# Performance work log

Measured on AMD Instinct MI355X. Metric: run time of the kernel, lower is better.

Reference implementation:

```python
import jax, jax.numpy as jnp
import numpy as np

B, T, N, D, H, C = 128, 128, 16, 128, 128, 4096
LEAKY_SLOPE = 0.2  # tf.nn.leaky_relu default alpha


def setup_inputs() -> dict:
    key = jax.random.key(0)
    ks = jax.random.split(key, 16)
    def p(k, shape, scale=0.05):
        return jax.random.normal(k, shape, dtype=jnp.float32) * scale
    return {
        "x_embed": jax.random.normal(ks[0], (B, T, D), dtype=jnp.float32),
        "spat_neigh": jax.random.normal(ks[1], (B, T, N, D), dtype=jnp.float32),
        "temp_neigh": jax.random.normal(ks[2], (B, T, N, D), dtype=jnp.float32),
        # spatial GAT params: shared projection w (no bias), attentionDense (2D->D, bias)
        "s_w": p(ks[3], (D, D)), "s_ak": p(ks[4], (2 * D, D)), "s_ab": jnp.zeros((D,), jnp.float32),
        # temporal GAT params
        "t_w": p(ks[5], (D, D)), "t_ak": p(ks[6], (2 * D, D)), "t_ab": jnp.zeros((D,), jnp.float32),
        # LSTMCell: W(x), U(h)+bias, s_W(spatial), t_W(temporal), each -> 4H
        "Wx": p(ks[7], (D, 4 * H)), "Uh": p(ks[8], (H, 4 * H)), "Ub": jnp.zeros((4 * H,), jnp.float32),
        "sW": p(ks[9], (D, 4 * H)), "tW": p(ks[10], (D, 4 * H)),
        # fuseDense -> num_classes
        "Wf": p(ks[11], (H, C)), "bf": jnp.zeros((C,), jnp.float32),
    }


def _gat(x, neigh, w, ak, ab):
    # x: [B,T,D], neigh: [B,T,N,D]
    px = x @ w                                   # projected main node [B,T,D]
    pn = neigh @ w                               # projected neighbours [B,T,N,D]
    cat = jnp.concatenate(
        [jnp.broadcast_to(px[:, :, None, :], pn.shape), pn], axis=-1)  # [B,T,N,2D]
    e = jax.nn.leaky_relu(cat @ ak + ab, negative_slope=LEAKY_SLOPE)   # [B,T,N,D]
    a = jax.nn.softmax(e, axis=2)                # softmax over neighbour axis
    return jnp.sum(a * pn, axis=2)               # [B,T,D]


def reference(x_embed, spat_neigh, temp_neigh,
              s_w, s_ak, s_ab, t_w, t_ak, t_ab,
              Wx, Uh, Ub, sW, tW, Wf, bf):
    spatial = _gat(x_embed, spat_neigh, s_w, s_ak, s_ab)   # [B,T,D]
    temporal = _gat(x_embed, temp_neigh, t_w, t_ak, t_ab)  # [B,T,D]

    # precompute non-recurrent gate preactivations for all timesteps
    pre = x_embed @ Wx + spatial @ sW + temporal @ tW + Ub  # [B,T,4H]
    pre_t = jnp.transpose(pre, (1, 0, 2))                   # [T,B,4H]

    def step(carry, p):
        h, c = carry
        g = p + h @ Uh                                      # [B,4H]
        i_g, f_g, o_g, c_g = jnp.split(g, 4, axis=-1)
        c = jax.nn.sigmoid(f_g) * c + jax.nn.sigmoid(i_g) * jnp.tanh(c_g)
        h = jnp.tanh(jax.nn.sigmoid(o_g) * c)  # nonstandard: tanh(o * c), per source
        return (h, c), h

    init = (jnp.zeros((B, H), jnp.float32), jnp.zeros((B, H), jnp.float32))
    _, hs = jax.lax.scan(step, init, pre_t)                 # [T,B,H]
    outputs = jnp.transpose(hs, (1, 0, 2))                  # [B,T,H]
    return outputs @ Wf + bf                                # [B,T,C] logits
```

## Files before the change

### kernel.cpp

```cpp
#include <hip/hip_runtime.h>
#include <hip/hip_bf16.h>
#include <math.h>

#define BT   16384
#define CC   4096

typedef __attribute__((ext_vector_type(8))) short short8v;
typedef __attribute__((ext_vector_type(8))) unsigned short ushort8v;
typedef __attribute__((ext_vector_type(4))) float f32x4;
typedef __attribute__((ext_vector_type(2))) _Float16 h2v;

__device__ __forceinline__ unsigned short f2bf(float f) {
  union { float f; unsigned int u; } v; v.f = f;
  unsigned int r = (v.u + 0x7fffu + ((v.u >> 16) & 1u)) >> 16;
  return (unsigned short)r;
}

__device__ __forceinline__ float fsig(float x) {
  return 1.0f / (1.0f + __expf(-x));
}
__device__ __forceinline__ float ftanh(float x) {
  return 1.0f - 2.0f / (__expf(2.0f * x) + 1.0f);
}

__device__ __forceinline__ float dot2f(float hbits, unsigned int ubits,
                                       float acc) {
#if __has_builtin(__builtin_amdgcn_fdot2)
  h2v ha = __builtin_bit_cast(h2v, hbits);
  h2v ub = __builtin_bit_cast(h2v, ubits);
  return __builtin_amdgcn_fdot2(ha, ub, acc, false);
#else
  union { unsigned int u; _Float16 h[2]; } A, B;
  A.u = __builtin_bit_cast(unsigned int, hbits);
  B.u = ubits;
  return acc + (float)A.h[0] * (float)B.h[0] + (float)A.h[1] * (float)B.h[1];
#endif
}

__global__ __launch_bounds__(128) void prep_dots_kernel(
    const float* __restrict__ s_w, const float* __restrict__ s_ak,
    const float* __restrict__ s_ab, const float* __restrict__ t_w,
    const float* __restrict__ t_ak, const float* __restrict__ t_ab,
    unsigned short* __restrict__ wqT, unsigned short* __restrict__ wcT,
    float* __restrict__ abp) {
  int d = blockIdx.x, quad = blockIdx.y;
  int g = quad & 1;
  const float* w  = g ? t_w  : s_w;
  const float* ak = g ? t_ak : s_ak;
  int akoff = (quad >> 1) ? 128 : 0;
  __shared__ float akcol[128];
  int k = threadIdx.x;
  akcol[k] = ak[(akoff + k) * 128 + d];
  if (quad < 2) {
    wcT[g * 32768 + d * 128 + k] = f2bf(w[k * 128 + d]);
    if (k == 0) abp[g * 128 + d] = g ? t_ab[d] : s_ab[d];
  }
  __syncthreads();
  float acc = 0.f;
  #pragma unroll 8
  for (int m = 0; m < 128; ++m) acc = fmaf(w[k * 128 + m], akcol[m], acc);
  if (quad < 2) wqT[(g * 128 + d) * 128 + k] = f2bf(acc);
  else          wcT[g * 32768 + (128 + d) * 128 + k] = f2bf(acc);
}

__global__ __launch_bounds__(256) void prep_wfT_kernel(
    const float* __restrict__ Wf, unsigned short* __restrict__ WfT) {
  __shared__ float tile[32][33];
  int n0 = blockIdx.x * 32, k0 = blockIdx.y * 32;
  int c = threadIdx.x & 31, r0 = threadIdx.x >> 5;
  #pragma unroll
  for (int i = 0; i < 4; ++i) {
    int r = r0 + i * 8;
    tile[r][c] = Wf[(size_t)(k0 + r) * 4096 + n0 + c];
  }
  __syncthreads();
  #pragma unroll
  for (int i = 0; i < 4; ++i) {
    int r = r0 + i * 8;
    WfT[(size_t)(n0 + r) * 128 + k0 + c] = f2bf(tile[c][r]);
  }
}

__global__ __launch_bounds__(256) void tconv_kernel(
    const float* __restrict__ s0, const float* __restrict__ s1,
    const float* __restrict__ s2, unsigned short* __restrict__ d0,
    unsigned short* __restrict__ d1, unsigned short* __restrict__ d2, int N) {
  int z = blockIdx.z;
  const float* src = (z == 0) ? s0 : (z == 1) ? s1 : s2;
  unsigned short* dst = (z == 0) ? d0 : (z == 1) ? d1 : d2;
  __shared__ float tile[32][33];
  int n0 = blockIdx.x * 32, k0 = blockIdx.y * 32;
  int c = threadIdx.x & 31, r0 = threadIdx.x >> 5;
  #pragma unroll
  for (int i = 0; i < 4; ++i) {
    int r = r0 + i * 8;
    tile[r][c] = src[(size_t)(k0 + r) * N + n0 + c];
  }
  __syncthreads();
  #pragma unroll
  for (int i = 0; i < 4; ++i) {
    int r = r0 + i * 8;
    dst[(size_t)(n0 + r) * 128 + k0 + c] = f2bf(tile[c][r]);
  }
}

__global__ __launch_bounds__(256) void uhconv_kernel(
    const float* __restrict__ Uh, unsigned int* __restrict__ UhH) {
  int idx = blockIdx.x * 256 + threadIdx.x;
  int k2 = idx >> 9, j = idx & 511;
  float a = Uh[(size_t)(2 * k2) * 512 + j];
  float b = Uh[(size_t)(2 * k2 + 1) * 512 + j];
  union { _Float16 h[2]; unsigned int u; } p;
  p.h[0] = (_Float16)a;
  p.h[1] = (_Float16)b;
  UhH[idx] = p.u;
}

__global__ __launch_bounds__(256) void xconv_kernel(
    const float* __restrict__ x, unsigned short* __restrict__ xb) {
  int i = blockIdx.x * 256 + threadIdx.x;
  const float4* x4 = (const float4*)x;
  float4 a = x4[(size_t)i * 2], b = x4[(size_t)i * 2 + 1];
  ushort8v v;
  v[0] = f2bf(a.x); v[1] = f2bf(a.y); v[2] = f2bf(a.z); v[3] = f2bf(a.w);
  v[4] = f2bf(b.x); v[5] = f2bf(b.y); v[6] = f2bf(b.z); v[7] = f2bf(b.w);
  *(ushort8v*)(xb + (size_t)i * 8) = v;
}

__global__ __launch_bounds__(256) void mfma_gemm_kernel(
    const unsigned short* __restrict__ A, const unsigned short* __restrict__ BTm,
    const float* __restrict__ bias, float* __restrict__ C, int N) {
  __shared__ unsigned short As[128 * 128];
  __shared__ unsigned short Bs[64 * 128];
  int tid = threadIdx.x;
  int m0 = blockIdx.x * 128, n0 = blockIdx.y * 64;
  #pragma unroll
  for (int i = 0; i < 8; ++i) {
    int cix = i * 256 + tid, row = cix >> 4, ch = cix & 15;
    ushort8v v = *(const ushort8v*)(A + (size_t)(m0 + row) * 128 + ch * 8);
    *(ushort8v*)&As[row * 128 + ((ch ^ (row & 7)) << 3)] = v;
  }
  #pragma unroll
  for (int i = 0; i < 4; ++i) {
    int cix = i * 256 + tid, row = cix >> 4, ch = cix & 15;
    ushort8v v = *(const ushort8v*)(BTm + (size_t)(n0 + row) * 128 + ch * 8);
    *(ushort8v*)&Bs[row * 128 + ((ch ^ (row & 7)) << 3)] = v;
  }
  __syncthreads();
  int lane = tid & 63, w = tid >> 6;
  int col = lane & 15, grp = lane >> 4;

  f32x4 acc[2][4];
  #pragma unroll
  for (int tm = 0; tm < 2; ++tm)
    #pragma unroll
    for (int tn = 0; tn < 4; ++tn) acc[tm][tn] = (f32x4){0.f, 0.f, 0.f, 0.f};

  #pragma unroll
  for (int kk = 0; kk < 4; ++kk) {
    int ch = kk * 4 + grp;
    short8v af[2], bf[4];
    #pragma unroll
    for (int tm = 0; tm < 2; ++tm) {
      int row = w * 32 + tm * 16 + col;
      af[tm] = *(const short8v*)&As[row * 128 + ((ch ^ (row & 7)) << 3)];
    }
    #pragma unroll
    for (int tn = 0; tn < 4; ++tn) {
      int row = tn * 16 + col;
      bf[tn] = *(const short8v*)&Bs[row * 128 + ((ch ^ (row & 7)) << 3)];
    }
    #pragma unroll
    for (int tm = 0; tm < 2; ++tm)
      #pragma unroll
      for (int tn = 0; tn < 4; ++tn)
        acc[tm][tn] = __builtin_amdgcn_mfma_f32_16x16x32_bf16(af[tm], bf[tn],
                                                              acc[tm][tn], 0, 0, 0);
  }

  #pragma unroll
  for (int tm = 0; tm < 2; ++tm)
    #pragma unroll
    for (int tn = 0; tn < 4; ++tn) {
      int cg = n0 + tn * 16 + col;
      float bv = bias[cg];
      int rbase = m0 + w * 32 + tm * 16 + grp * 4;
      #pragma unroll
      for (int r = 0; r < 4; ++r)
        C[(size_t)(rbase + r) * N + cg] = acc[tm][tn][r] + bv;
    }
}

__global__ __launch_bounds__(256) void mfma_gemm3_kernel(
    const unsigned short* __restrict__ A0, const unsigned short* __restrict__ A1,
    const unsigned short* __restrict__ A2, const unsigned short* __restrict__ B0,
    const unsigned short* __restrict__ B1, const unsigned short* __restrict__ B2,
    int nmat, const float* __restrict__ bias, float* __restrict__ C, int N) {
  __shared__ unsigned short As[128 * 128];
  __shared__ unsigned short Bs[64 * 128];
  int tid = threadIdx.x;
  int m0 = blockIdx.x * 128, n0 = blockIdx.y * 64;
  int lane = tid & 63, w = tid >> 6;
  int col = lane & 15, grp = lane >> 4;

  f32x4 acc[2][4];
  #pragma unroll
  for (int tm = 0; tm < 2; ++tm)
    #pragma unroll
    for (int tn = 0; tn < 4; ++tn) acc[tm][tn] = (f32x4){0.f, 0.f, 0.f, 0.f};

  for (int s = 0; s < nmat; ++s) {
    const unsigned short* A   = (s == 0) ? A0 : (s == 1) ? A1 : A2;
    const unsigned short* BTm = (s == 0) ? B0 : (s == 1) ? B1 : B2;
    if (s) __syncthreads();
    #pragma unroll
    for (int i = 0; i < 8; ++i) {
      int cix = i * 256 + tid, row = cix >> 4, ch = cix & 15;
      ushort8v v = *(const ushort8v*)(A + (size_t)(m0 + row) * 128 + ch * 8);
      *(ushort8v*)&As[row * 128 + ((ch ^ (row & 7)) << 3)] = v;
    }
    #pragma unroll
    for (int i = 0; i < 4; ++i) {
      int cix = i * 256 + tid, row = cix >> 4, ch = cix & 15;
      ushort8v v = *(const ushort8v*)(BTm + (size_t)(n0 + row) * 128 + ch * 8);
      *(ushort8v*)&Bs[row * 128 + ((ch ^ (row & 7)) << 3)] = v;
    }
    __syncthreads();

    #pragma unroll
    for (int kk = 0; kk < 4; ++kk) {
      int ch = kk * 4 + grp;
      short8v af[2], bf[4];
      #pragma unroll
      for (int tm = 0; tm < 2; ++tm) {
        int row = w * 32 + tm * 16 + col;
        af[tm] = *(const short8v*)&As[row * 128 + ((ch ^ (row & 7)) << 3)];
      }
      #pragma unroll
      for (int tn = 0; tn < 4; ++tn) {
        int row = tn * 16 + col;
        bf[tn] = *(const short8v*)&Bs[row * 128 + ((ch ^ (row & 7)) << 3)];
      }
      #pragma unroll
      for (int tm = 0; tm < 2; ++tm)
        #pragma unroll
        for (int tn = 0; tn < 4; ++tn)
          acc[tm][tn] = __builtin_amdgcn_mfma_f32_16x16x32_bf16(
              af[tm], bf[tn], acc[tm][tn], 0, 0, 0);
    }
  }

  #pragma unroll
  for (int tm = 0; tm < 2; ++tm)
    #pragma unroll
    for (int tn = 0; tn < 4; ++tn) {
      int cg = n0 + tn * 16 + col;
      float bv = bias[cg];
      int rbase = m0 + w * 32 + tm * 16 + grp * 4;
      #pragma unroll
      for (int r = 0; r < 4; ++r)
        C[(size_t)(rbase + r) * N + cg] = acc[tm][tn][r] + bv;
    }
}

__global__ __launch_bounds__(256) void gat_mfma_kernel(
    const float* __restrict__ sneigh, const float* __restrict__ tneigh,
    const unsigned short* __restrict__ wcT, const float* __restrict__ qb,
    unsigned short* __restrict__ spb, unsigned short* __restrict__ tpb) {
  int g = blockIdx.y;
  const float* neigh = g ? tneigh : sneigh;
  const unsigned short* wc = wcT + g * 32768;
  unsigned short* outp = g ? tpb : spb;

  __shared__ unsigned short Bsh[256 * 128];
  int tid = threadIdx.x;
  #pragma unroll
  for (int i = 0; i < 16; ++i) {
    int cix = i * 256 + tid, row = cix >> 4, ch = cix & 15;
    ushort8v v = *(const ushort8v*)(wc + row * 128 + ch * 8);
    *(ushort8v*)&Bsh[row * 128 + ((ch ^ (row & 7)) << 3)] = v;
  }
  __syncthreads();

  int lane = tid & 63, wid = tid >> 6;
  int col = lane & 15, grp = lane >> 4;

  const int NIT = 8;
  int btbase = blockIdx.x * (4 * NIT) + wid * NIT;

  float4 bufA[8], bufB[8];
  float qA[8], qB[8];

  auto load_bt = [&](int bt, float4 (&fa)[8], float (&qv)[8]) {
    const float* nb = neigh + ((size_t)bt * 16 + col) * 128 + grp * 8;
    #pragma unroll
    for (int kk = 0; kk < 4; ++kk) {
      fa[2 * kk]     = *(const float4*)(nb + kk * 32);
      fa[2 * kk + 1] = *(const float4*)(nb + kk * 32 + 4);
    }
    const float* qrow = qb + (size_t)bt * 256 + g * 128 + col;
    #pragma unroll
    for (int t = 0; t < 8; ++t) qv[t] = qrow[t * 16];
  };

  auto step = [&](int bt, int btn, float4 (&cur)[8], float (&qc)[8],
                  float4 (&nxt)[8], float (&qn)[8]) {
    load_bt(btn, nxt, qn);

    short8v af[4];
    #pragma unroll
    for (int kk = 0; kk < 4; ++kk) {
      float4 a = cur[2 * kk], b = cur[2 * kk + 1];
      short8v t;
      t[0] = (short)f2bf(a.x); t[1] = (short)f2bf(a.y);
      t[2] = (short)f2bf(a.z); t[3] = (short)f2bf(a.w);
      t[4] = (short)f2bf(b.x); t[5] = (short)f2bf(b.y);
      t[6] = (short)f2bf(b.z); t[7] = (short)f2bf(b.w);
      af[kk] = t;
    }

    f32x4 acc[16];
    #pragma unroll
    for (int nt = 0; nt < 16; ++nt) acc[nt] = (f32x4){0.f, 0.f, 0.f, 0.f};

    #pragma unroll
    for (int kk = 0; kk < 4; ++kk) {
      int ch = kk * 4 + grp;
      #pragma unroll
      for (int nt = 0; nt < 16; ++nt) {
        int row = nt * 16 + col;
        short8v bfv = *(const short8v*)&Bsh[row * 128 + ((ch ^ (row & 7)) << 3)];
        acc[nt] = __builtin_amdgcn_mfma_f32_16x16x32_bf16(af[kk], bfv, acc[nt],
                                                          0, 0, 0);
      }
    }

    #pragma unroll
    for (int t = 0; t < 8; ++t) {
      float qvv = qc[t];
      float e0 = qvv + acc[8 + t][0], e1 = qvv + acc[8 + t][1];
      float e2 = qvv + acc[8 + t][2], e3 = qvv + acc[8 + t][3];
      e0 = (e0 > 0.f) ? e0 : 0.2f * e0;
      e1 = (e1 > 0.f) ? e1 : 0.2f * e1;
      e2 = (e2 > 0.f) ? e2 : 0.2f * e2;
      e3 = (e3 > 0.f) ? e3 : 0.2f * e3;
      float mx = fmaxf(fmaxf(e0, e1), fmaxf(e2, e3));
      mx = fmaxf(mx, __shfl_xor(mx, 16));
      mx = fmaxf(mx, __shfl_xor(mx, 32));
      float p0 = __expf(e0 - mx), p1 = __expf(e1 - mx);
      float p2 = __expf(e2 - mx), p3 = __expf(e3 - mx);
      float s = p0 + p1 + p2 + p3;
      float o = p0 * acc[t][0] + p1 * acc[t][1] + p2 * acc[t][2] + p3 * acc[t][3];
      s += __shfl_xor(s, 16); s += __shfl_xor(s, 32);
      o += __shfl_xor(o, 16); o += __shfl_xor(o, 32);
      if (grp == (t & 3)) outp[(size_t)bt * 128 + t * 16 + col] = f2bf(o / s);
    }
  };

  load_bt(btbase, bufA, qA);
  #pragma unroll
  for (int p = 0; p < NIT / 2; ++p) {
    int bt = btbase + 2 * p;
    int b2 = (bt + 2 < BT) ? bt + 2 : bt;
    step(bt, bt + 1, bufA, qA, bufB, qB);
    step(bt + 1, b2, bufB, qB, bufA, qA);
  }
}

__global__ __launch_bounds__(512, 2) void lstm_kernel(
    const float* __restrict__ pre, const unsigned int* __restrict__ UhH,
    unsigned short* __restrict__ hsb) {
  int b = blockIdx.x;
  int j = threadIdx.x;
  __shared__ _Float16 hh[128];
  __shared__ float nl_lds[512];
  unsigned int u2[64];
  #pragma unroll
  for (int k2 = 0; k2 < 64; ++k2) u2[k2] = UhH[k2 * 512 + j];
  float c = 0.f;
  if (j < 128) hh[j] = (_Float16)0.f;
  __syncthreads();
  const float4* hv4 = (const float4*)hh;
  const float* prow = pre + (size_t)b * 128 * 512 + j;
  unsigned short* hrow = hsb + (size_t)b * 128 * 128 + (j & 127);
  float pcur = prow[0];
  for (int t = 0; t < 128; ++t) {
    float pnext = (t < 127) ? prow[(size_t)(t + 1) * 512] : 0.f;

    float ga = pcur, gb = 0.f, gc = 0.f, gd = 0.f;
    #pragma unroll
    for (int i = 0; i < 4; ++i) {
      float4 v0 = hv4[i * 4 + 0];
      float4 v1 = hv4[i * 4 + 1];
      float4 v2 = hv4[i * 4 + 2];
      float4 v3 = hv4[i * 4 + 3];
      int kb = i * 16;
      ga = dot2f(v0.x, u2[kb + 0], ga);
      gb = dot2f(v0.y, u2[kb + 1], gb);
      gc = dot2f(v0.z, u2[kb + 2], gc);
      gd = dot2f(v0.w, u2[kb + 3], gd);
      ga = dot2f(v1.x, u2[kb + 4], ga);
      gb = dot2f(v1.y, u2[kb + 5], gb);
      gc = dot2f(v1.z, u2[kb + 6], gc);
      gd = dot2f(v1.w, u2[kb + 7], gd);
      ga = dot2f(v2.x, u2[kb + 8], ga);
      gb = dot2f(v2.y, u2[kb + 9], gb);
      gc = dot2f(v2.z, u2[kb + 10], gc);
      gd = dot2f(v2.w, u2[kb + 11], gd);
      ga = dot2f(v3.x, u2[kb + 12], ga);
      gb = dot2f(v3.y, u2[kb + 13], gb);
      gc = dot2f(v3.z, u2[kb + 14], gc);
      gd = dot2f(v3.w, u2[kb + 15], gd);
    }
    float g = (ga + gb) + (gc + gd);

    float nl = (j < 384) ? fsig(g) : ftanh(g);
    nl_lds[j] = nl;
    __syncthreads();

    if (j < 128) {
      float ig = nl_lds[j], fg = nl_lds[j + 128];
      float og = nl_lds[j + 256], cg = nl_lds[j + 384];
      c = fg * c + ig * cg;
      float h = ftanh(og * c);
      hh[j] = (_Float16)h;
      hrow[(size_t)t * 128] = f2bf(h);
    }
    __syncthreads();
    pcur = pnext;
  }
}

extern "C" void kernel_launch(void* const* d_in, const int* in_sizes, int n_in,
                              void* d_out, int out_size, void* d_ws,
                              size_t ws_size, hipStream_t stream) {
  const float* x    = (const float*)d_in[0];
  const float* sn   = (const float*)d_in[1];
  const float* tn   = (const float*)d_in[2];
  const float* s_w  = (const float*)d_in[3];
  const float* s_ak = (const float*)d_in[4];
  const float* s_ab = (const float*)d_in[5];
  const float* t_w  = (const float*)d_in[6];
  const float* t_ak = (const float*)d_in[7];
  const float* t_ab = (const float*)d_in[8];
  const float* Wx   = (const float*)d_in[9];
  const float* Uh   = (const float*)d_in[10];
  const float* Ub   = (const float*)d_in[11];
  const float* sW   = (const float*)d_in[12];
  const float* tW   = (const float*)d_in[13];
  const float* Wf   = (const float*)d_in[14];
  const float* bfb  = (const float*)d_in[15];
  float* out = (float*)d_out;

  unsigned short* wqT = (unsigned short*)d_ws;
  unsigned short* wcT = (unsigned short*)((char*)d_ws + 65536);
  unsigned short* WfT = (unsigned short*)((char*)d_ws + 196608);
  unsigned short* hsb = (unsigned short*)((char*)d_ws + 1245184);
  float*          abp = (float*)((char*)d_ws + 5439488);

  float* pre = out;
  float* q   = out + 12582912;
  unsigned short* xb  = (unsigned short*)(out + 16777216);
  unsigned short* spb = (unsigned short*)(out + 17825792);
  unsigned short* tpb = (unsigned short*)(out + 18874368);
  unsigned short* WxT = (unsigned short*)(out + 19922944);
  unsigned short* sWT = (unsigned short*)(out + 19955712);
  unsigned short* tWT = (unsigned short*)(out + 19988480);
  unsigned int*   UhH = (unsigned int*)(out + 20054016);

  prep_dots_kernel<<<dim3(128, 4), 128, 0, stream>>>(s_w, s_ak, s_ab, t_w, t_ak,
                                                     t_ab, wqT, wcT, abp);
  prep_wfT_kernel<<<dim3(128, 4), 256, 0, stream>>>(Wf, WfT);
  tconv_kernel<<<dim3(16, 4, 3), 256, 0, stream>>>(Wx, sW, tW, WxT, sWT, tWT,
                                                   512);
  uhconv_kernel<<<128, 256, 0, stream>>>(Uh, UhH);
  xconv_kernel<<<1024, 256, 0, stream>>>(x, xb);
  mfma_gemm_kernel<<<dim3(128, 4), 256, 0, stream>>>(xb, wqT, abp, q, 256);
  gat_mfma_kernel<<<dim3(512, 2), 256, 0, stream>>>(sn, tn, wcT, q, spb, tpb);
  mfma_gemm3_kernel<<<dim3(128, 8), 256, 0, stream>>>(xb, spb, tpb, WxT, sWT,
                                                      tWT, 3, Ub, pre, 512);
  lstm_kernel<<<128, 512, 0, stream>>>(pre, UhH, hsb);
  mfma_gemm_kernel<<<dim3(128, 64), 256, 0, stream>>>(hsb, WfT, bfb, out, CC);
}
```

Baseline: 302.4 us.

## Halve LSTM block size, two gate columns per thread

The LSTM recurrence kernel now runs 256 threads per batch row instead of 512. Each thread computes two gate columns (i and o for the low threads, f and c for the high threads), so the i and o gates stay in registers and only f and c pass through shared memory. This cuts barrier participants, halves the LDS broadcast reads of h per gate, and adds instruction-level parallelism. In exchange each thread holds 128 Uh registers, which raises register pressure and risks spills.

```diff
diff --git a/kernel.cpp b/kernel.cpp
--- a/kernel.cpp
+++ b/kernel.cpp
@@ -367,27 +367,38 @@
   }
 }
 
-__global__ __launch_bounds__(512, 2) void lstm_kernel(
+__global__ __launch_bounds__(256, 2) void lstm_kernel(
     const float* __restrict__ pre, const unsigned int* __restrict__ UhH,
     unsigned short* __restrict__ hsb) {
   int b = blockIdx.x;
-  int j = threadIdx.x;
+  int tid = threadIdx.x;
+  int c0 = tid, c1 = tid + 256;
   __shared__ _Float16 hh[128];
-  __shared__ float nl_lds[512];
-  unsigned int u2[64];
-  #pragma unroll
-  for (int k2 = 0; k2 < 64; ++k2) u2[k2] = UhH[k2 * 512 + j];
-  float c = 0.f;
-  if (j < 128) hh[j] = (_Float16)0.f;
+  __shared__ float nl_f[128];
+  __shared__ float nl_c[128];
+  unsigned int u0[64], u1[64];
+  #pragma unroll
+  for (int k2 = 0; k2 < 64; ++k2) {
+    u0[k2] = UhH[k2 * 512 + c0];
+    u1[k2] = UhH[k2 * 512 + c1];
+  }
+  float cc = 0.f;
+  if (tid < 128) hh[tid] = (_Float16)0.f;
   __syncthreads();
   const float4* hv4 = (const float4*)hh;
-  const float* prow = pre + (size_t)b * 128 * 512 + j;
-  unsigned short* hrow = hsb + (size_t)b * 128 * 128 + (j & 127);
-  float pcur = prow[0];
+  const float* prow = pre + (size_t)b * 128 * 512;
+  unsigned short* hrow = hsb + (size_t)b * 128 * 128 + tid;
+  float p0 = prow[c0], p1 = prow[c1];
   for (int t = 0; t < 128; ++t) {
-    float pnext = (t < 127) ? prow[(size_t)(t + 1) * 512] : 0.f;
-
-    float ga = pcur, gb = 0.f, gc = 0.f, gd = 0.f;
+    float pn0 = 0.f, pn1 = 0.f;
+    if (t < 127) {
+      const float* pnx = prow + (size_t)(t + 1) * 512;
+      pn0 = pnx[c0];
+      pn1 = pnx[c1];
+    }
+
+    float a0 = p0, b0 = 0.f, g0c = 0.f, d0 = 0.f;
+    float a1 = p1, b1 = 0.f, g1c = 0.f, d1 = 0.f;
     #pragma unroll
     for (int i = 0; i < 4; ++i) {
       float4 v0 = hv4[i * 4 + 0];
@@ -395,39 +406,45 @@
       float4 v2 = hv4[i * 4 + 2];
       float4 v3 = hv4[i * 4 + 3];
       int kb = i * 16;
-      ga = dot2f(v0.x, u2[kb + 0], ga);
-      gb = dot2f(v0.y, u2[kb + 1], gb);
-      gc = dot2f(v0.z, u2[kb + 2], gc);
-      gd = dot2f(v0.w, u2[kb + 3], gd);
-      ga = dot2f(v1.x, u2[kb + 4], ga);
-      gb = dot2f(v1.y, u2[kb + 5], gb);
-      gc = dot2f(v1.z, u2[kb + 6], gc);
-      gd = dot2f(v1.w, u2[kb + 7], gd);
-      ga = dot2f(v2.x, u2[kb + 8], ga);
-      gb = dot2f(v2.y, u2[kb + 9], gb);
-      gc = dot2f(v2.z, u2[kb + 10], gc);
-      gd = dot2f(v2.w, u2[kb + 11], gd);
-      ga = dot2f(v3.x, u2[kb + 12], ga);
-      gb = dot2f(v3.y, u2[kb + 13], gb);
-      gc = dot2f(v3.z, u2[kb + 14], gc);
-      gd = dot2f(v3.w, u2[kb + 15], gd);
-    }
-    float g = (ga + gb) + (gc + gd);
-
-    float nl = (j < 384) ? fsig(g) : ftanh(g);
-    nl_lds[j] = nl;
+      a0 = dot2f(v0.x, u0[kb + 0], a0);  a1 = dot2f(v0.x, u1[kb + 0], a1);
+      b0 = dot2f(v0.y, u0[kb + 1], b0);  b1 = dot2f(v0.y, u1[kb + 1], b1);
+      g0c = dot2f(v0.z, u0[kb + 2], g0c); g1c = dot2f(v0.z, u1[kb + 2], g1c);
+      d0 = dot2f(v0.w, u0[kb + 3], d0);  d1 = dot2f(v0.w, u1[kb + 3], d1);
+      a0 = dot2f(v1.x, u0[kb + 4], a0);  a1 = dot2f(v1.x, u1[kb + 4], a1);
+      b0 = dot2f(v1.y, u0[kb + 5], b0);  b1 = dot2f(v1.y, u1[kb + 5], b1);
+      g0c = dot2f(v1.z, u0[kb + 6], g0c); g1c = dot2f(v1.z, u1[kb + 6], g1c);
+      d0 = dot2f(v1.w, u0[kb + 7], d0);  d1 = dot2f(v1.w, u1[kb + 7], d1);
+      a0 = dot2f(v2.x, u0[kb + 8], a0);  a1 = dot2f(v2.x, u1[kb + 8], a1);
+      b0 = dot2f(v2.y, u0[kb + 9], b0);  b1 = dot2f(v2.y, u1[kb + 9], b1);
+      g0c = dot2f(v2.z, u0[kb + 10], g0c); g1c = dot2f(v2.z, u1[kb + 10], g1c);
+      d0 = dot2f(v2.w, u0[kb + 11], d0);  d1 = dot2f(v2.w, u1[kb + 11], d1);
+      a0 = dot2f(v3.x, u0[kb + 12], a0);  a1 = dot2f(v3.x, u1[kb + 12], a1);
+      b0 = dot2f(v3.y, u0[kb + 13], b0);  b1 = dot2f(v3.y, u1[kb + 13], b1);
+      g0c = dot2f(v3.z, u0[kb + 14], g0c); g1c = dot2f(v3.z, u1[kb + 14], g1c);
+      d0 = dot2f(v3.w, u0[kb + 15], d0);  d1 = dot2f(v3.w, u1[kb + 15], d1);
+    }
+    float g0 = (a0 + b0) + (g0c + d0);
+    float g1 = (a1 + b1) + (g1c + d1);
+
+    float nl0 = fsig(g0);
+    float nl1 = (tid < 128) ? fsig(g1) : ftanh(g1);
+    if (tid >= 128) {
+      nl_f[tid - 128] = nl0;
+      nl_c[tid - 128] = nl1;
+    }
     __syncthreads();
 
-    if (j < 128) {
-      float ig = nl_lds[j], fg = nl_lds[j + 128];
-      float og = nl_lds[j + 256], cg = nl_lds[j + 384];
-      c = fg * c + ig * cg;
-      float h = ftanh(og * c);
-      hh[j] = (_Float16)h;
+    if (tid < 128) {
+      float ig = nl0, og = nl1;
+      float fg = nl_f[tid], cg = nl_c[tid];
+      cc = fg * cc + ig * cg;
+      float h = ftanh(og * cc);
+      hh[tid] = (_Float16)h;
       hrow[(size_t)t * 128] = f2bf(h);
     }
     __syncthreads();
-    pcur = pnext;
+    p0 = pn0;
+    p1 = pn1;
   }
 }
 
@@ -479,6 +496,6 @@
   gat_mfma_kernel<<<dim3(512, 2), 256, 0, stream>>>(sn, tn, wcT, q, spb, tpb);
   mfma_gemm3_kernel<<<dim3(128, 8), 256, 0, stream>>>(xb, spb, tpb, WxT, sWT,
                                                       tWT, 3, Ub, pre, 512);
-  lstm_kernel<<<128, 512, 0, stream>>>(pre, UhH, hsb);
+  lstm_kernel<<<128, 256, 0, stream>>>(pre, UhH, hsb);
   mfma_gemm_kernel<<<dim3(128, 64), 256, 0, stream>>>(hsb, WfT, bfb, out, CC);
 }
```

Result: no change. 306.6 us (+1.4%).

## Process two neighbour rows per MFMA pass sharing LDS B-fragment loads

Applied to the files above, without the earlier changes.

The GAT attention kernel now handles two (b,t) positions together, so each B-fragment read from shared memory feeds two MFMAs instead of one, halving LDS traffic per MFMA. The 16 output tiles are split into two halves so accumulator registers stay bounded, and neighbour loads for the next pair are prefetched into a single raw buffer while the current pair computes. This raises register pressure and drops the full loop unroll, which may reduce occupancy or overlap.

```diff
diff --git a/kernel.cpp b/kernel.cpp
--- a/kernel.cpp
+++ b/kernel.cpp
@@ -285,85 +285,113 @@
   int lane = tid & 63, wid = tid >> 6;
   int col = lane & 15, grp = lane >> 4;
 
-  const int NIT = 8;
-  int btbase = blockIdx.x * (4 * NIT) + wid * NIT;
-
-  float4 bufA[8], bufB[8];
-  float qA[8], qB[8];
-
-  auto load_bt = [&](int bt, float4 (&fa)[8], float (&qv)[8]) {
+  int btbase = blockIdx.x * 32 + wid * 8;
+
+  float4 raw[16];
+  short8v af[2][4];
+
+  auto load_pair = [&](int bt) {
     const float* nb = neigh + ((size_t)bt * 16 + col) * 128 + grp * 8;
     #pragma unroll
     for (int kk = 0; kk < 4; ++kk) {
-      fa[2 * kk]     = *(const float4*)(nb + kk * 32);
-      fa[2 * kk + 1] = *(const float4*)(nb + kk * 32 + 4);
-    }
-    const float* qrow = qb + (size_t)bt * 256 + g * 128 + col;
-    #pragma unroll
-    for (int t = 0; t < 8; ++t) qv[t] = qrow[t * 16];
+      raw[2 * kk]     = *(const float4*)(nb + kk * 32);
+      raw[2 * kk + 1] = *(const float4*)(nb + kk * 32 + 4);
+    }
+    const float* nb1 = nb + 2048;
+    #pragma unroll
+    for (int kk = 0; kk < 4; ++kk) {
+      raw[8 + 2 * kk]     = *(const float4*)(nb1 + kk * 32);
+      raw[8 + 2 * kk + 1] = *(const float4*)(nb1 + kk * 32 + 4);
+    }
   };
 
-  auto step = [&](int bt, int btn, float4 (&cur)[8], float (&qc)[8],
-                  float4 (&nxt)[8], float (&qn)[8]) {
-    load_bt(btn, nxt, qn);
-
-    short8v af[4];
-    #pragma unroll
-    for (int kk = 0; kk < 4; ++kk) {
-      float4 a = cur[2 * kk], b = cur[2 * kk + 1];
-      short8v t;
-      t[0] = (short)f2bf(a.x); t[1] = (short)f2bf(a.y);
-      t[2] = (short)f2bf(a.z); t[3] = (short)f2bf(a.w);
-      t[4] = (short)f2bf(b.x); t[5] = (short)f2bf(b.y);
-      t[6] = (short)f2bf(b.z); t[7] = (short)f2bf(b.w);
-      af[kk] = t;
-    }
-
-    f32x4 acc[16];
-    #pragma unroll
-    for (int nt = 0; nt < 16; ++nt) acc[nt] = (f32x4){0.f, 0.f, 0.f, 0.f};
-
-    #pragma unroll
-    for (int kk = 0; kk < 4; ++kk) {
-      int ch = kk * 4 + grp;
-      #pragma unroll
-      for (int nt = 0; nt < 16; ++nt) {
-        int row = nt * 16 + col;
-        short8v bfv = *(const short8v*)&Bsh[row * 128 + ((ch ^ (row & 7)) << 3)];
-        acc[nt] = __builtin_amdgcn_mfma_f32_16x16x32_bf16(af[kk], bfv, acc[nt],
-                                                          0, 0, 0);
+  auto cvt_pair = [&]() {
+    #pragma unroll
+    for (int bb = 0; bb < 2; ++bb)
+      #pragma unroll
+      for (int kk = 0; kk < 4; ++kk) {
+        float4 a = raw[bb * 8 + 2 * kk], b = raw[bb * 8 + 2 * kk + 1];
+        short8v t;
+        t[0] = (short)f2bf(a.x); t[1] = (short)f2bf(a.y);
+        t[2] = (short)f2bf(a.z); t[3] = (short)f2bf(a.w);
+        t[4] = (short)f2bf(b.x); t[5] = (short)f2bf(b.y);
+        t[6] = (short)f2bf(b.z); t[7] = (short)f2bf(b.w);
+        af[bb][kk] = t;
       }
-    }
-
-    #pragma unroll
-    for (int t = 0; t < 8; ++t) {
-      float qvv = qc[t];
-      float e0 = qvv + acc[8 + t][0], e1 = qvv + acc[8 + t][1];
-      float e2 = qvv + acc[8 + t][2], e3 = qvv + acc[8 + t][3];
-      e0 = (e0 > 0.f) ? e0 : 0.2f * e0;
-      e1 = (e1 > 0.f) ? e1 : 0.2f * e1;
-      e2 = (e2 > 0.f) ? e2 : 0.2f * e2;
-      e3 = (e3 > 0.f) ? e3 : 0.2f * e3;
-      float mx = fmaxf(fmaxf(e0, e1), fmaxf(e2, e3));
-      mx = fmaxf(mx, __shfl_xor(mx, 16));
-      mx = fmaxf(mx, __shfl_xor(mx, 32));
-      float p0 = __expf(e0 - mx), p1 = __expf(e1 - mx);
-      float p2 = __expf(e2 - mx), p3 = __expf(e3 - mx);
-      float s = p0 + p1 + p2 + p3;
-      float o = p0 * acc[t][0] + p1 * acc[t][1] + p2 * acc[t][2] + p3 * acc[t][3];
-      s += __shfl_xor(s, 16); s += __shfl_xor(s, 32);
-      o += __shfl_xor(o, 16); o += __shfl_xor(o, 32);
-      if (grp == (t & 3)) outp[(size_t)bt * 128 + t * 16 + col] = f2bf(o / s);
-    }
   };
 
-  load_bt(btbase, bufA, qA);
-  #pragma unroll
-  for (int p = 0; p < NIT / 2; ++p) {
+  load_pair(btbase);
+  cvt_pair();
+
+  for (int p = 0; p < 4; ++p) {
     int bt = btbase + 2 * p;
-    int b2 = (bt + 2 < BT) ? bt + 2 : bt;
-    step(bt, bt + 1, bufA, qA, bufB, qB);
-    step(bt + 1, b2, bufB, qB, bufA, qA);
+    int btn = (p < 3) ? bt + 2 : bt;
+
+    float qv[2][8];
+    {
+      const float* qrow = qb + (size_t)bt * 256 + g * 128 + col;
+      #pragma unroll
+      for (int t = 0; t < 8; ++t) {
+        qv[0][t] = qrow[t * 16];
+        qv[1][t] = qrow[256 + t * 16];
+      }
+    }
+
+    load_pair(btn);
+
+    #pragma unroll
+    for (int hf = 0; hf < 2; ++hf) {
+      f32x4 acc[2][8];
+      #pragma unroll
+      for (int bb = 0; bb < 2; ++bb)
+        #pragma unroll
+        for (int j = 0; j < 8; ++j) acc[bb][j] = (f32x4){0.f, 0.f, 0.f, 0.f};
+
+      #pragma unroll
+      for (int kk = 0; kk < 4; ++kk) {
+        int ch = kk * 4 + grp;
+        #pragma unroll
+        for (int j = 0; j < 8; ++j) {
+          int nt = (j < 4) ? (hf * 4 + j) : (4 + hf * 4 + j);
+          int row = nt * 16 + col;
+          short8v bfv =
+              *(const short8v*)&Bsh[row * 128 + ((ch ^ (row & 7)) << 3)];
+          acc[0][j] = __builtin_amdgcn_mfma_f32_16x16x32_bf16(af[0][kk], bfv,
+                                                              acc[0][j], 0, 0, 0);
+          acc[1][j] = __builtin_amdgcn_mfma_f32_16x16x32_bf16(af[1][kk], bfv,
+                                                              acc[1][j], 0, 0, 0);
+        }
+      }
+
+      #pragma unroll
+      for (int bb = 0; bb < 2; ++bb) {
+        #pragma unroll
+        for (int tj = 0; tj < 4; ++tj) {
+          int t = hf * 4 + tj;
+          float qvv = qv[bb][t];
+          float e0 = qvv + acc[bb][4 + tj][0], e1 = qvv + acc[bb][4 + tj][1];
+          float e2 = qvv + acc[bb][4 + tj][2], e3 = qvv + acc[bb][4 + tj][3];
+          e0 = (e0 > 0.f) ? e0 : 0.2f * e0;
+          e1 = (e1 > 0.f) ? e1 : 0.2f * e1;
+          e2 = (e2 > 0.f) ? e2 : 0.2f * e2;
+          e3 = (e3 > 0.f) ? e3 : 0.2f * e3;
+          float mx = fmaxf(fmaxf(e0, e1), fmaxf(e2, e3));
+          mx = fmaxf(mx, __shfl_xor(mx, 16));
+          mx = fmaxf(mx, __shfl_xor(mx, 32));
+          float p0 = __expf(e0 - mx), p1 = __expf(e1 - mx);
+          float p2 = __expf(e2 - mx), p3 = __expf(e3 - mx);
+          float s = p0 + p1 + p2 + p3;
+          float o = p0 * acc[bb][tj][0] + p1 * acc[bb][tj][1] +
+                    p2 * acc[bb][tj][2] + p3 * acc[bb][tj][3];
+          s += __shfl_xor(s, 16); s += __shfl_xor(s, 32);
+          o += __shfl_xor(o, 16); o += __shfl_xor(o, 32);
+          if (grp == (t & 3))
+            outp[(size_t)(bt + bb) * 128 + t * 16 + col] = f2bf(o / s);
+        }
+      }
+    }
+
+    cvt_pair();
   }
 }
 
```

After: 350.7 us. 16.0% more time.
